# Kernel tuning notes

Measured on AMD Instinct MI355X. Metric: run time of the kernel, lower is better.

## Reference

```python
import jax, jax.numpy as jnp
import numpy as np

D_MODEL = 2048
N_HEADS = 32
N_KV_HEADS = 8
D_K = D_MODEL // N_HEADS          # 64
N_REP = N_HEADS // N_KV_HEADS     # 4
KV_DIM = N_KV_HEADS * D_K         # 512
B, T = 4, 2048


def setup_inputs() -> dict:
    key = jax.random.key(0)
    ks = jax.random.split(key, 9)
    s_in = 1.0 / np.sqrt(D_MODEL)
    x = jax.random.normal(ks[0], (B, T, D_MODEL), dtype=jnp.float32)
    Wq = jax.random.uniform(ks[1], (D_MODEL, D_MODEL), jnp.float32, -s_in, s_in)
    bq = jax.random.uniform(ks[2], (D_MODEL,), jnp.float32, -s_in, s_in)
    Wk = jax.random.uniform(ks[3], (D_MODEL, KV_DIM), jnp.float32, -s_in, s_in)
    bk = jax.random.uniform(ks[4], (KV_DIM,), jnp.float32, -s_in, s_in)
    Wv = jax.random.uniform(ks[5], (D_MODEL, KV_DIM), jnp.float32, -s_in, s_in)
    bv = jax.random.uniform(ks[6], (KV_DIM,), jnp.float32, -s_in, s_in)
    Wo = jax.random.uniform(ks[7], (D_MODEL, D_MODEL), jnp.float32, -s_in, s_in)
    bo = jax.random.uniform(ks[8], (D_MODEL,), jnp.float32, -s_in, s_in)
    return {"x": x, "Wq": Wq, "bq": bq, "Wk": Wk, "bk": bk,
            "Wv": Wv, "bv": bv, "Wo": Wo, "bo": bo}


def reference(x, Wq, bq, Wk, bk, Wv, bv, Wo, bo):
    Bsz, S, _ = x.shape
    # projections
    q = x @ Wq + bq                                   # (B, T, d_model)
    k = x @ Wk + bk                                   # (B, T, kv_dim)
    v = x @ Wv + bv
    # (B, n_kv, n_rep, T, d_k) for q; (B, n_kv, T, d_k) for k, v.
    # Grouping q by kv head avoids materializing repeated K/V.
    q = q.reshape(Bsz, S, N_KV_HEADS, N_REP, D_K).transpose(0, 2, 3, 1, 4)
    k = k.reshape(Bsz, S, N_KV_HEADS, D_K).transpose(0, 2, 1, 3)
    v = v.reshape(Bsz, S, N_KV_HEADS, D_K).transpose(0, 2, 1, 3)
    scale = 1.0 / np.sqrt(D_K).astype(np.float32)
    scores = jnp.einsum('bgrtd,bgsd->bgrts', q, k) * scale  # (B, n_kv, n_rep, T, T)
    causal = jnp.tril(jnp.ones((S, S), dtype=bool))
    scores = jnp.where(causal, scores, jnp.finfo(scores.dtype).min)
    p = jax.nn.softmax(scores, axis=-1)
    o = jnp.einsum('bgrts,bgsd->bgrtd', p, v)               # (B, n_kv, n_rep, T, d_k)
    o = o.transpose(0, 3, 1, 2, 4).reshape(Bsz, S, D_MODEL)
    return o @ Wo + bo
```

## Files before the change

kernel.cpp:

```cpp
#include <hip/hip_runtime.h>
#include <cstdint>
#include <cstddef>

typedef __attribute__((ext_vector_type(8))) short short8;
typedef __attribute__((ext_vector_type(4))) float f32x4;

#define D_MODEL 2048
#define KV_DIM  512
#define N_HEADS 32
#define N_KV    8
#define D_K     64
#define B_SZ    4
#define T_SEQ   2048
#define M_TOT   (B_SZ * T_SEQ)
#define N1      (D_MODEL + 2 * KV_DIM)
#define NEG_BIG (-1e30f)

__device__ __forceinline__ unsigned short f2bf(float f) {
    union { float f; unsigned int i; } c; c.f = f;
    unsigned int u = c.i;
    u += 0x7FFFu + ((u >> 16) & 1u);
    return (unsigned short)(u >> 16);
}

__global__ __launch_bounds__(256)
void stage_x(const float* __restrict__ x, unsigned short* __restrict__ xb, int n) {
    for (int i = blockIdx.x * blockDim.x + threadIdx.x; i * 4 < n;
         i += gridDim.x * blockDim.x) {
        const f32x4 v = *(const f32x4*)&x[i * 4];
        unsigned short o[4];
#pragma unroll
        for (int k = 0; k < 4; k++) o[k] = f2bf(v[k]);
        *(uint64_t*)&xb[i * 4] = *(const uint64_t*)o;
    }
}

__global__ __launch_bounds__(256)
void transpose_f32_bf16(const float* __restrict__ src,
                        unsigned short* __restrict__ dst, int R, int C) {
    __shared__ unsigned short tile[32][34];
    int bx = blockIdx.x * 32;
    int by = blockIdx.y * 32;
    int tx = threadIdx.x;
    int ty = threadIdx.y;
#pragma unroll
    for (int i = 0; i < 32; i += 8)
        tile[ty + i][tx] = f2bf(src[(size_t)(by + ty + i) * C + bx + tx]);
    __syncthreads();
#pragma unroll
    for (int i = 0; i < 32; i += 8)
        dst[(size_t)(bx + ty + i) * R + by + tx] = tile[tx][ty + i];
}

template <int MODE>
__global__ __launch_bounds__(256)
void gemm_bt(const unsigned short* __restrict__ A,
             const unsigned short* __restrict__ Bt,
             const float* __restrict__ b0,
             const float* __restrict__ b1,
             const float* __restrict__ b2,
             unsigned short* __restrict__ out0,
             unsigned short* __restrict__ out1,
             unsigned short* __restrict__ out2,
             float* __restrict__ outF,
             int K) {
    __shared__ __align__(16) unsigned short As[128 * 32];
    __shared__ __align__(16) unsigned short Bs[128 * 32];

    const int t    = threadIdx.x;
    const int wave = t >> 6;
    const int lane = t & 63;
    const int quad = lane >> 4;
    const int l16  = lane & 15;
    const int wm   = (wave >> 1) * 64;
    const int wn   = (wave & 1) * 64;
    const int rowBase = blockIdx.y * 128;
    const int colBase = blockIdx.x * 128;

    f32x4 acc[4][4];
#pragma unroll
    for (int i = 0; i < 4; i++)
#pragma unroll
        for (int j = 0; j < 4; j++)
            acc[i][j] = (f32x4){0.f, 0.f, 0.f, 0.f};

    const int r0  = t >> 2;
    const int off = (t & 3) * 8;
    const unsigned short* Ap = A  + (size_t)(rowBase + r0) * K + off;
    const unsigned short* Bp = Bt + (size_t)(colBase + r0) * K + off;
    const size_t rowStep = (size_t)64 * K;

    for (int k0 = 0; k0 < K; k0 += 32) {
        *(short8*)&As[t * 8]         = *(const short8*)(Ap + k0);
        *(short8*)&As[(t + 256) * 8] = *(const short8*)(Ap + rowStep + k0);
        *(short8*)&Bs[t * 8]         = *(const short8*)(Bp + k0);
        *(short8*)&Bs[(t + 256) * 8] = *(const short8*)(Bp + rowStep + k0);
        __syncthreads();

        short8 af[4], bfr[4];
#pragma unroll
        for (int i = 0; i < 4; i++)
            af[i] = *(const short8*)&As[(wm + i * 16 + l16) * 32 + quad * 8];
#pragma unroll
        for (int i = 0; i < 4; i++)
            bfr[i] = *(const short8*)&Bs[(wn + i * 16 + l16) * 32 + quad * 8];

#pragma unroll
        for (int mi = 0; mi < 4; mi++)
#pragma unroll
            for (int ni = 0; ni < 4; ni++)
                acc[mi][ni] = __builtin_amdgcn_mfma_f32_16x16x32_bf16(
                    af[mi], bfr[ni], acc[mi][ni], 0, 0, 0);
        __syncthreads();
    }

#pragma unroll
    for (int mi = 0; mi < 4; mi++) {
        const int rowT = rowBase + wm + mi * 16 + quad * 4;
#pragma unroll
        for (int ni = 0; ni < 4; ni++) {
            const int col = colBase + wn + ni * 16 + l16;
#pragma unroll
            for (int r = 0; r < 4; r++) {
                float v = acc[mi][ni][r];
                const int rr = rowT + r;
                if (MODE == 0) {
                    if (col < D_MODEL) {
                        v += b0[col];
                        out0[(size_t)rr * D_MODEL + col] = f2bf(v);
                    } else if (col < D_MODEL + KV_DIM) {
                        const int c = col - D_MODEL;
                        v += b1[c];
                        out1[(size_t)rr * KV_DIM + c] = f2bf(v);
                    } else {
                        const int c = col - (D_MODEL + KV_DIM);
                        v += b2[c];
                        const int b   = rr >> 11;
                        const int tt  = rr & 2047;
                        const int kvh = c >> 6;
                        const int d   = c & 63;
                        out2[((size_t)((b * N_KV + kvh) * D_K + d)) * T_SEQ + tt] = f2bf(v);
                    }
                } else {
                    v += b0[col];
                    outF[(size_t)rr * D_MODEL + col] = v;
                }
            }
        }
    }
}

__global__ __launch_bounds__(256)
void attn_fwd(const unsigned short* __restrict__ qb,
              const unsigned short* __restrict__ kb,
              const unsigned short* __restrict__ vt,
              unsigned short* __restrict__ ob) {
    __shared__ __align__(16) unsigned short Ks[64 * 72];
    __shared__ __align__(16) unsigned short Vs[64 * 72];
    __shared__ __align__(16) unsigned short Ps[128 * 72];

    const int t    = threadIdx.x;
    const int wave = t >> 6;
    const int lane = t & 63;
    const int quad = lane >> 4;
    const int l16  = lane & 15;
    const int qt   = blockIdx.x;
    const int h    = blockIdx.y;
    const int b    = blockIdx.z;
    const int kvh  = h >> 2;
    const int qBase = qt * 128;
    const int rowG  = b * T_SEQ;

    short8 qf[2][2];
#pragma unroll
    for (int mi = 0; mi < 2; mi++) {
        const int row = rowG + qBase + wave * 32 + mi * 16 + l16;
#pragma unroll
        for (int kk = 0; kk < 2; kk++)
            qf[mi][kk] = *(const short8*)&qb[(size_t)row * D_MODEL + h * D_K + kk * 32 + quad * 8];
    }

    f32x4 oacc[2][4];
#pragma unroll
    for (int i = 0; i < 2; i++)
#pragma unroll
        for (int j = 0; j < 4; j++)
            oacc[i][j] = (f32x4){0.f, 0.f, 0.f, 0.f};
    float m_run[2][4], l_run[2][4];
#pragma unroll
    for (int i = 0; i < 2; i++)
#pragma unroll
        for (int r = 0; r < 4; r++) { m_run[i][r] = NEG_BIG; l_run[i][r] = 0.f; }

    const float scale = 0.125f;
    const int jMax = 2 * qt + 1;

    for (int j = 0; j <= jMax; ++j) {
        const int sBase = j * 64;
        __syncthreads();

#pragma unroll
        for (int i = 0; i < 2; i++) {
            const int c = t + i * 256;
            const int r = c >> 3, o = (c & 7) * 8;
            *(short8*)&Ks[r * 72 + o] =
                *(const short8*)&kb[(size_t)(rowG + sBase + r) * KV_DIM + kvh * D_K + o];
            *(short8*)&Vs[r * 72 + o] =
                *(const short8*)&vt[(size_t)((b * N_KV + kvh) * D_K + r) * T_SEQ + sBase + o];
        }
        __syncthreads();

        f32x4 sacc[2][4];
#pragma unroll
        for (int ni = 0; ni < 4; ni++) {
            const short8 kf0 = *(const short8*)&Ks[(ni * 16 + l16) * 72 + quad * 8];
            const short8 kf1 = *(const short8*)&Ks[(ni * 16 + l16) * 72 + 32 + quad * 8];
#pragma unroll
            for (int mi = 0; mi < 2; mi++) {
                f32x4 s = (f32x4){0.f, 0.f, 0.f, 0.f};
                s = __builtin_amdgcn_mfma_f32_16x16x32_bf16(qf[mi][0], kf0, s, 0, 0, 0);
                s = __builtin_amdgcn_mfma_f32_16x16x32_bf16(qf[mi][1], kf1, s, 0, 0, 0);
                sacc[mi][ni] = s;
            }
        }

        const bool diag = (j >= 2 * qt);
        const int  sRel = sBase - qBase;
#pragma unroll
        for (int mi = 0; mi < 2; mi++) {
            float tm[4];
#pragma unroll
            for (int r = 0; r < 4; r++) tm[r] = NEG_BIG;
#pragma unroll
            for (int ni = 0; ni < 4; ni++) {
#pragma unroll
                for (int r = 0; r < 4; r++) {
                    float v = sacc[mi][ni][r] * scale;
                    if (diag) {
                        const int qrow = wave * 32 + mi * 16 + quad * 4 + r;
                        const int scol = sRel + ni * 16 + l16;
                        if (scol > qrow) v = NEG_BIG;
                    }
                    sacc[mi][ni][r] = v;
                    tm[r] = fmaxf(tm[r], v);
                }
            }
#pragma unroll
            for (int r = 0; r < 4; r++) {
                float v = tm[r];
                v = fmaxf(v, __shfl_xor(v, 1));
                v = fmaxf(v, __shfl_xor(v, 2));
                v = fmaxf(v, __shfl_xor(v, 4));
                v = fmaxf(v, __shfl_xor(v, 8));
                const float mnew  = fmaxf(m_run[mi][r], v);
                const float alpha = __expf(m_run[mi][r] - mnew);
                m_run[mi][r] = mnew;
                l_run[mi][r] *= alpha;
#pragma unroll
                for (int di = 0; di < 4; di++) oacc[mi][di][r] *= alpha;
                float rs = 0.f;
#pragma unroll
                for (int ni = 0; ni < 4; ni++) {
                    const float p = __expf(sacc[mi][ni][r] - mnew);
                    sacc[mi][ni][r] = p;
                    rs += p;
                }
                rs += __shfl_xor(rs, 1);
                rs += __shfl_xor(rs, 2);
                rs += __shfl_xor(rs, 4);
                rs += __shfl_xor(rs, 8);
                l_run[mi][r] += rs;
            }
#pragma unroll
            for (int ni = 0; ni < 4; ni++)
#pragma unroll
                for (int r = 0; r < 4; r++)
                    Ps[(wave * 32 + mi * 16 + quad * 4 + r) * 72 + ni * 16 + l16] =
                        f2bf(sacc[mi][ni][r]);
        }
        __syncthreads();

#pragma unroll
        for (int ks = 0; ks < 2; ++ks) {
            short8 pa[2];
#pragma unroll
            for (int mi = 0; mi < 2; mi++)
                pa[mi] = *(const short8*)&Ps[(wave * 32 + mi * 16 + l16) * 72 + ks * 32 + quad * 8];
#pragma unroll
            for (int di = 0; di < 4; ++di) {
                const short8 vb = *(const short8*)&Vs[(di * 16 + l16) * 72 + ks * 32 + quad * 8];
#pragma unroll
                for (int mi = 0; mi < 2; mi++)
                    oacc[mi][di] = __builtin_amdgcn_mfma_f32_16x16x32_bf16(
                        pa[mi], vb, oacc[mi][di], 0, 0, 0);
            }
        }
    }

#pragma unroll
    for (int mi = 0; mi < 2; mi++) {
#pragma unroll
        for (int r = 0; r < 4; r++) {
            const float inv = 1.f / l_run[mi][r];
            const int row = rowG + qBase + wave * 32 + mi * 16 + quad * 4 + r;
#pragma unroll
            for (int di = 0; di < 4; di++)
                ob[(size_t)row * D_MODEL + h * D_K + di * 16 + l16] =
                    f2bf(oacc[mi][di][r] * inv);
        }
    }
}

extern "C" void kernel_launch(void* const* d_in, const int* in_sizes, int n_in,
                              void* d_out, int out_size, void* d_ws, size_t ws_size,
                              hipStream_t stream) {
    const float* x  = (const float*)d_in[0];
    const float* Wq = (const float*)d_in[1];
    const float* bq = (const float*)d_in[2];
    const float* Wk = (const float*)d_in[3];
    const float* bk = (const float*)d_in[4];
    const float* Wv = (const float*)d_in[5];
    const float* bv = (const float*)d_in[6];
    const float* Wo = (const float*)d_in[7];
    const float* bo = (const float*)d_in[8];
    float* out = (float*)d_out;

    char* ws = (char*)d_ws;
    unsigned short* qb   = (unsigned short*)(ws);
    unsigned short* Wbuf = (unsigned short*)(ws + 33554432);
    unsigned short* xb   = (unsigned short*)(ws + 46137344);
    unsigned short* kb   = (unsigned short*)d_out;
    unsigned short* vt   = (unsigned short*)d_out + 4194304;

    stage_x<<<4096, 256, 0, stream>>>(x, xb, 16777216);

    dim3 tb(32, 8);
    transpose_f32_bf16<<<dim3(64, 64), tb, 0, stream>>>(Wq, Wbuf, 2048, 2048);
    transpose_f32_bf16<<<dim3(16, 64), tb, 0, stream>>>(Wk, Wbuf + 2048 * 2048, 2048, 512);
    transpose_f32_bf16<<<dim3(16, 64), tb, 0, stream>>>(Wv, Wbuf + 2560 * 2048, 2048, 512);

    gemm_bt<0><<<dim3(N1 / 128, M_TOT / 128), 256, 0, stream>>>(
        xb, Wbuf, bq, bk, bv, qb, kb, vt, nullptr, D_MODEL);

    transpose_f32_bf16<<<dim3(64, 64), tb, 0, stream>>>(Wo, Wbuf, 2048, 2048);

    attn_fwd<<<dim3(T_SEQ / 128, N_HEADS, B_SZ), 256, 0, stream>>>(qb, kb, vt, qb);

    gemm_bt<1><<<dim3(D_MODEL / 128, M_TOT / 128), 256, 0, stream>>>(
        qb, Wbuf, bo, nullptr, nullptr, nullptr, nullptr, nullptr, out, D_MODEL);
}
```

Before: 870.2 us.

## Pipeline attention K/V loads via async LDS double buffering and register-resident P

Restructures the flash-attention kernel: K/V tiles are double-buffered in LDS using async global-to-LDS loads with an XOR swizzle. It computes S transposed so each lane holds a full query row, which cuts the softmax reductions to two shuffles. P is kept in registers as packed bf16 and redistributed by lane shuffles instead of going through LDS. It also adds lazy max rescaling with a threshold, reverses the query-tile order to start the longest causal blocks first, skips fully masked waves on the last tile, and raises wave priority around the MFMA sections. This should hide load latency and remove barriers, at the cost of many shuffles, more complexity, and a lazy-rescale trick that relies on bounded exp growth.

```diff
diff --git a/kernel.cpp b/kernel.cpp
--- a/kernel.cpp
+++ b/kernel.cpp
@@ -21,6 +21,18 @@
     unsigned int u = c.i;
     u += 0x7FFFu + ((u >> 16) & 1u);
     return (unsigned short)(u >> 16);
+}
+
+__device__ __forceinline__ unsigned int cvtpk_bf16(float lo, float hi) {
+    unsigned int r;
+    asm("v_cvt_pk_bf16_f32 %0, %1, %2" : "=v"(r) : "v"(lo), "v"(hi));
+    return r;
+}
+
+__device__ __forceinline__ void async16(unsigned short* lds, const unsigned short* g) {
+    __builtin_amdgcn_global_load_lds(
+        (const __attribute__((address_space(1))) unsigned int*)g,
+        (__attribute__((address_space(3))) unsigned int*)lds, 16, 0, 0);
 }
 
 __global__ __launch_bounds__(256)
@@ -155,21 +167,21 @@
               const unsigned short* __restrict__ kb,
               const unsigned short* __restrict__ vt,
               unsigned short* __restrict__ ob) {
-    __shared__ __align__(16) unsigned short Ks[64 * 72];
-    __shared__ __align__(16) unsigned short Vs[64 * 72];
-    __shared__ __align__(16) unsigned short Ps[128 * 72];
+    __shared__ __align__(16) unsigned short Ks[2][64 * 64];
+    __shared__ __align__(16) unsigned short Vs[2][64 * 64];
 
     const int t    = threadIdx.x;
     const int wave = t >> 6;
     const int lane = t & 63;
     const int quad = lane >> 4;
     const int l16  = lane & 15;
-    const int qt   = blockIdx.x;
+    const int qt   = (int)gridDim.x - 1 - (int)blockIdx.x;
     const int h    = blockIdx.y;
     const int b    = blockIdx.z;
     const int kvh  = h >> 2;
     const int qBase = qt * 128;
     const int rowG  = b * T_SEQ;
+    const size_t vtBase = (size_t)(b * N_KV + kvh) * D_K * T_SEQ;
 
     short8 qf[2][2];
 #pragma unroll
@@ -186,122 +198,159 @@
 #pragma unroll
         for (int j = 0; j < 4; j++)
             oacc[i][j] = (f32x4){0.f, 0.f, 0.f, 0.f};
-    float m_run[2][4], l_run[2][4];
-#pragma unroll
-    for (int i = 0; i < 2; i++)
-#pragma unroll
-        for (int r = 0; r < 4; r++) { m_run[i][r] = NEG_BIG; l_run[i][r] = 0.f; }
+    float m_run[2], l_run[2];
+#pragma unroll
+    for (int i = 0; i < 2; i++) { m_run[i] = NEG_BIG; l_run[i] = 0.f; }
+
+    const int rr  = t >> 3;
+    const int sc8 = ((t & 7) ^ (rr & 7)) << 3;
+
+    auto stage = [&](int bi, int sB) {
+#pragma unroll
+        for (int i = 0; i < 2; i++) {
+            const int row = i * 32 + rr;
+            async16(&Ks[bi][(i * 32 + wave * 8) * 64],
+                    kb + (size_t)(rowG + sB + row) * KV_DIM + kvh * D_K + sc8);
+            async16(&Vs[bi][(i * 32 + wave * 8) * 64],
+                    vt + vtBase + (size_t)row * T_SEQ + sB + sc8);
+        }
+    };
 
     const float scale = 0.125f;
     const int jMax = 2 * qt + 1;
+    int buf = 0;
+
+    stage(0, 0);
+    __syncthreads();
 
     for (int j = 0; j <= jMax; ++j) {
-        const int sBase = j * 64;
-        __syncthreads();
-
-#pragma unroll
-        for (int i = 0; i < 2; i++) {
-            const int c = t + i * 256;
-            const int r = c >> 3, o = (c & 7) * 8;
-            *(short8*)&Ks[r * 72 + o] =
-                *(const short8*)&kb[(size_t)(rowG + sBase + r) * KV_DIM + kvh * D_K + o];
-            *(short8*)&Vs[r * 72 + o] =
-                *(const short8*)&vt[(size_t)((b * N_KV + kvh) * D_K + r) * T_SEQ + sBase + o];
-        }
-        __syncthreads();
-
-        f32x4 sacc[2][4];
-#pragma unroll
-        for (int ni = 0; ni < 4; ni++) {
-            const short8 kf0 = *(const short8*)&Ks[(ni * 16 + l16) * 72 + quad * 8];
-            const short8 kf1 = *(const short8*)&Ks[(ni * 16 + l16) * 72 + 32 + quad * 8];
+        if (j < jMax) stage(buf ^ 1, (j + 1) * 64);
+
+        if (!(j == jMax && wave < 2)) {
+            const int sBase = j * 64;
+            const bool diag = (j >= 2 * qt);
+            const int sRel  = sBase - qBase;
+            const char* KsB = (const char*)&Ks[buf][0];
+            const char* VsB = (const char*)&Vs[buf][0];
+            const int swz   = (l16 & 7) << 4;
+
+            f32x4 sacc[4][2];
+            __builtin_amdgcn_s_setprio(1);
+#pragma unroll
+            for (int ni = 0; ni < 4; ni++) {
+                const int rowB = (ni * 16 + l16) * 128;
+                const short8 kf0 = *(const short8*)(KsB + rowB + ((quad * 16) ^ swz));
+                const short8 kf1 = *(const short8*)(KsB + rowB + ((64 + quad * 16) ^ swz));
+#pragma unroll
+                for (int mi = 0; mi < 2; mi++) {
+                    f32x4 s = (f32x4){0.f, 0.f, 0.f, 0.f};
+                    s = __builtin_amdgcn_mfma_f32_16x16x32_bf16(kf0, qf[mi][0], s, 0, 0, 0);
+                    s = __builtin_amdgcn_mfma_f32_16x16x32_bf16(kf1, qf[mi][1], s, 0, 0, 0);
+                    sacc[ni][mi] = s;
+                }
+            }
+            __builtin_amdgcn_s_setprio(0);
+
+            uint2 packed[4][2];
 #pragma unroll
             for (int mi = 0; mi < 2; mi++) {
-                f32x4 s = (f32x4){0.f, 0.f, 0.f, 0.f};
-                s = __builtin_amdgcn_mfma_f32_16x16x32_bf16(qf[mi][0], kf0, s, 0, 0, 0);
-                s = __builtin_amdgcn_mfma_f32_16x16x32_bf16(qf[mi][1], kf1, s, 0, 0, 0);
-                sacc[mi][ni] = s;
+                float tm = NEG_BIG;
+#pragma unroll
+                for (int ni = 0; ni < 4; ni++)
+#pragma unroll
+                    for (int r = 0; r < 4; r++) {
+                        float v = sacc[ni][mi][r] * scale;
+                        if (diag) {
+                            const int kc = sRel + ni * 16 + quad * 4 + r;
+                            const int qr = wave * 32 + mi * 16 + l16;
+                            if (kc > qr) v = NEG_BIG;
+                        }
+                        sacc[ni][mi][r] = v;
+                        tm = fmaxf(tm, v);
+                    }
+                tm = fmaxf(tm, __shfl_xor(tm, 16));
+                tm = fmaxf(tm, __shfl_xor(tm, 32));
+
+                float mref = m_run[mi];
+                float mnew, alpha;
+                if (__all(tm <= mref + 8.f)) {
+                    mnew = mref; alpha = 1.f;
+                } else {
+                    mnew  = fmaxf(mref, tm);
+                    alpha = __expf(mref - mnew);
+                    m_run[mi] = mnew;
+#pragma unroll
+                    for (int r2 = 0; r2 < 4; r2++) {
+                        const float aR = __shfl(alpha, (lane & 48) + quad * 4 + r2);
+#pragma unroll
+                        for (int di = 0; di < 4; di++) oacc[mi][di][r2] *= aR;
+                    }
+                }
+                float rs = 0.f;
+#pragma unroll
+                for (int ni = 0; ni < 4; ni++) {
+#pragma unroll
+                    for (int r = 0; r < 4; r++) {
+                        const float p = __expf(sacc[ni][mi][r] - mnew);
+                        sacc[ni][mi][r] = p;
+                        rs += p;
+                    }
+                    packed[ni][mi].x = cvtpk_bf16(sacc[ni][mi][0], sacc[ni][mi][1]);
+                    packed[ni][mi].y = cvtpk_bf16(sacc[ni][mi][2], sacc[ni][mi][3]);
+                }
+                rs += __shfl_xor(rs, 16);
+                rs += __shfl_xor(rs, 32);
+                l_run[mi] = l_run[mi] * alpha + rs;
+            }
+
+#pragma unroll
+            for (int ks = 0; ks < 2; ks++) {
+                short8 pa[2];
+#pragma unroll
+                for (int mi = 0; mi < 2; mi++) {
+                    const int srcA = ((quad & 1) << 5) + l16;
+                    const uint2 pL = packed[2 * ks][mi];
+                    const uint2 pH = packed[2 * ks + 1][mi];
+                    const unsigned a0x = __shfl((int)pL.x, srcA);
+                    const unsigned a0y = __shfl((int)pL.y, srcA);
+                    const unsigned b0x = __shfl((int)pL.x, srcA + 16);
+                    const unsigned b0y = __shfl((int)pL.y, srcA + 16);
+                    const unsigned a1x = __shfl((int)pH.x, srcA);
+                    const unsigned a1y = __shfl((int)pH.y, srcA);
+                    const unsigned b1x = __shfl((int)pH.x, srcA + 16);
+                    const unsigned b1y = __shfl((int)pH.y, srcA + 16);
+                    const int hi = quad >> 1;
+                    union { unsigned u[4]; short8 s; } pw;
+                    pw.u[0] = hi ? a1x : a0x;
+                    pw.u[1] = hi ? a1y : a0y;
+                    pw.u[2] = hi ? b1x : b0x;
+                    pw.u[3] = hi ? b1y : b0y;
+                    pa[mi] = pw.s;
+                }
+                __builtin_amdgcn_s_setprio(1);
+#pragma unroll
+                for (int di = 0; di < 4; di++) {
+                    const short8 vb = *(const short8*)(VsB + (di * 16 + l16) * 128 +
+                                                      ((ks * 64 + quad * 16) ^ swz));
+#pragma unroll
+                    for (int mi = 0; mi < 2; mi++)
+                        oacc[mi][di] = __builtin_amdgcn_mfma_f32_16x16x32_bf16(
+                            pa[mi], vb, oacc[mi][di], 0, 0, 0);
+                }
+                __builtin_amdgcn_s_setprio(0);
             }
         }
 
-        const bool diag = (j >= 2 * qt);
-        const int  sRel = sBase - qBase;
-#pragma unroll
-        for (int mi = 0; mi < 2; mi++) {
-            float tm[4];
-#pragma unroll
-            for (int r = 0; r < 4; r++) tm[r] = NEG_BIG;
-#pragma unroll
-            for (int ni = 0; ni < 4; ni++) {
-#pragma unroll
-                for (int r = 0; r < 4; r++) {
-                    float v = sacc[mi][ni][r] * scale;
-                    if (diag) {
-                        const int qrow = wave * 32 + mi * 16 + quad * 4 + r;
-                        const int scol = sRel + ni * 16 + l16;
-                        if (scol > qrow) v = NEG_BIG;
-                    }
-                    sacc[mi][ni][r] = v;
-                    tm[r] = fmaxf(tm[r], v);
-                }
-            }
-#pragma unroll
-            for (int r = 0; r < 4; r++) {
-                float v = tm[r];
-                v = fmaxf(v, __shfl_xor(v, 1));
-                v = fmaxf(v, __shfl_xor(v, 2));
-                v = fmaxf(v, __shfl_xor(v, 4));
-                v = fmaxf(v, __shfl_xor(v, 8));
-                const float mnew  = fmaxf(m_run[mi][r], v);
-                const float alpha = __expf(m_run[mi][r] - mnew);
-                m_run[mi][r] = mnew;
-                l_run[mi][r] *= alpha;
-#pragma unroll
-                for (int di = 0; di < 4; di++) oacc[mi][di][r] *= alpha;
-                float rs = 0.f;
-#pragma unroll
-                for (int ni = 0; ni < 4; ni++) {
-                    const float p = __expf(sacc[mi][ni][r] - mnew);
-                    sacc[mi][ni][r] = p;
-                    rs += p;
-                }
-                rs += __shfl_xor(rs, 1);
-                rs += __shfl_xor(rs, 2);
-                rs += __shfl_xor(rs, 4);
-                rs += __shfl_xor(rs, 8);
-                l_run[mi][r] += rs;
-            }
-#pragma unroll
-            for (int ni = 0; ni < 4; ni++)
-#pragma unroll
-                for (int r = 0; r < 4; r++)
-                    Ps[(wave * 32 + mi * 16 + quad * 4 + r) * 72 + ni * 16 + l16] =
-                        f2bf(sacc[mi][ni][r]);
-        }
         __syncthreads();
-
-#pragma unroll
-        for (int ks = 0; ks < 2; ++ks) {
-            short8 pa[2];
-#pragma unroll
-            for (int mi = 0; mi < 2; mi++)
-                pa[mi] = *(const short8*)&Ps[(wave * 32 + mi * 16 + l16) * 72 + ks * 32 + quad * 8];
-#pragma unroll
-            for (int di = 0; di < 4; ++di) {
-                const short8 vb = *(const short8*)&Vs[(di * 16 + l16) * 72 + ks * 32 + quad * 8];
-#pragma unroll
-                for (int mi = 0; mi < 2; mi++)
-                    oacc[mi][di] = __builtin_amdgcn_mfma_f32_16x16x32_bf16(
-                        pa[mi], vb, oacc[mi][di], 0, 0, 0);
-            }
-        }
+        buf ^= 1;
     }
 
 #pragma unroll
     for (int mi = 0; mi < 2; mi++) {
 #pragma unroll
         for (int r = 0; r < 4; r++) {
-            const float inv = 1.f / l_run[mi][r];
+            const float lr  = __shfl(l_run[mi], (lane & 48) + quad * 4 + r);
+            const float inv = 1.f / lr;
             const int row = rowG + qBase + wave * 32 + mi * 16 + quad * 4 + r;
 #pragma unroll
             for (int di = 0; di < 4; di++)
```

New measurement: 751.3 us. 13.7% less time.
